# Kernel optimization log

Hardware: AMD Instinct MI355X
Metric: run time of the kernel (lower is better)

## Reference

```python
import jax, jax.numpy as jnp
import numpy as np

B, T, DC, DM, R = 64, 1000, 512, 80, 1
DP = 128          # prenet output dim
DH = 128          # prenet hidden dim
DA = 128          # attention hidden dim
DR = (1024, 1024) # decoder LSTM hidden dims
PZ = 0.1          # zoneout prob (eval-mode mixing)
PD = 0.5          # prenet dropout prob (always on)


def setup_inputs() -> dict:
    key = jax.random.key(0)
    ks = jax.random.split(key, 24)
    s = 0.02  # weight scale to keep activations in a sane range
    inp = {}
    inp['x'] = jax.random.normal(ks[0], (B, R, DM), jnp.float32)
    w = jax.random.uniform(ks[1], (B, T), jnp.float32)
    inp['w'] = w / jnp.sum(w, axis=1, keepdims=True)  # valid attention weights
    inp['h0'] = jax.random.normal(ks[2], (B, DR[0]), jnp.float32) * 0.1
    inp['c0'] = jax.random.normal(ks[3], (B, DR[0]), jnp.float32) * 0.1
    inp['h1'] = jax.random.normal(ks[4], (B, DR[1]), jnp.float32) * 0.1
    inp['c1'] = jax.random.normal(ks[5], (B, DR[1]), jnp.float32) * 0.1
    inp['memory'] = jax.random.normal(ks[6], (B, T, DC), jnp.float32)
    inp['mmask'] = jnp.ones((B, T), dtype=bool)
    inp['pre_w1'] = jax.random.normal(ks[7], (DM * R, DH), jnp.float32) * s
    inp['pre_b1'] = jnp.zeros((DH,), jnp.float32)
    inp['pre_w2'] = jax.random.normal(ks[8], (DH, DP), jnp.float32) * s
    inp['pre_b2'] = jnp.zeros((DP,), jnp.float32)
    inp['wih0'] = jax.random.normal(ks[9], (DP + DC, 4 * DR[0]), jnp.float32) * s
    inp['whh0'] = jax.random.normal(ks[10], (DR[0], 4 * DR[0]), jnp.float32) * s
    inp['b0'] = jnp.zeros((4 * DR[0],), jnp.float32)
    inp['wih1'] = jax.random.normal(ks[11], (DR[0] + DC, 4 * DR[1]), jnp.float32) * s
    inp['whh1'] = jax.random.normal(ks[12], (DR[1], 4 * DR[1]), jnp.float32) * s
    inp['b1'] = jnp.zeros((4 * DR[1],), jnp.float32)
    inp['att_wq'] = jax.random.normal(ks[13], (DR[0] + DR[1] + DC, DA), jnp.float32) * s
    inp['att_wm'] = jax.random.normal(ks[14], (DC, DA), jnp.float32) * s
    inp['att_b'] = jnp.zeros((DA,), jnp.float32)
    inp['att_v'] = jax.random.normal(ks[15], (DA,), jnp.float32) * s
    return inp


def _dropout(v, k, p):
    keep = jax.random.bernoulli(k, 1.0 - p, v.shape)
    return jnp.where(keep, v / (1.0 - p), 0.0)


def _lstm_zoneout(xi, h, c, wih, whh, b):
    # torch LSTMCell gate order: i, f, g, o
    g = xi @ wih + h @ whh + b
    i, f, gg, o = jnp.split(g, 4, axis=1)
    c_new = jax.nn.sigmoid(f) * c + jax.nn.sigmoid(i) * jnp.tanh(gg)
    h_new = jax.nn.sigmoid(o) * jnp.tanh(c_new)
    # eval-mode zoneout: expected-value mixing with previous state
    return (1.0 - PZ) * h_new + PZ * h, (1.0 - PZ) * c_new + PZ * c


def reference(x, w, h0, c0, h1, c1, memory, pre_w1, pre_b1, pre_w2, pre_b2,
              wih0, whh0, b0, wih1, whh1, b1, att_wq, att_wm, att_b, att_v, mmask):
    dk = jax.random.split(jax.random.key(42), 2)
    # PreNet (dropout always on, fixed keys for determinism)
    xf = x.reshape(x.shape[0], -1)                       # [B, r*dim_mel]
    h = _dropout(jax.nn.relu(xf @ pre_w1 + pre_b1), dk[0], PD)
    x_pre = _dropout(jax.nn.relu(h @ pre_w2 + pre_b2), dk[1], PD)  # [B, DP]
    # context = bmm(w, memory)
    ctx = jnp.einsum('bt,btc->bc', w, memory)            # [B, DC]
    # stacked zoneout LSTM cells with interleaved context concat
    h0n, c0n = _lstm_zoneout(jnp.concatenate([x_pre, ctx], axis=1), h0, c0, wih0, whh0, b0)
    h1n, c1n = _lstm_zoneout(jnp.concatenate([h0n, ctx], axis=1), h1, c1, wih1, whh1, b1)
    x_att = jnp.concatenate([h0n, h1n, jnp.zeros_like(ctx)], axis=1)  # [B, 2560]
    # stepwise monotonic attention: e = v.tanh(Wq q + Wm m + b); p = sigmoid(e)
    q = x_att @ att_wq                                   # [B, DA]
    proc = jnp.tanh(q[:, None, :] + jnp.einsum('btc,ca->bta', memory, att_wm) + att_b)
    e = jnp.einsum('bta,a->bt', proc, att_v)             # [B, T]
    e = jnp.where(mmask, e, -1e9)
    p = jax.nn.sigmoid(e)
    # alpha_j = alpha_j * p_j + alpha_{j-1} * (1 - p_{j-1})
    w_new = w * p + jnp.pad((w * (1.0 - p))[:, :-1], ((0, 0), (1, 0)))
    x_dec = jnp.concatenate([h0n, h1n, jnp.zeros_like(ctx)], axis=1)
    return x_dec, ctx, w_new, h0n, c0n, h1n, c1n
```

## Files before the change

### kernel.cpp

```cpp
#include <hip/hip_runtime.h>
#include <hip/hip_bf16.h>
#include <stdint.h>

#define B_  64
#define T_  1000
#define DC_ 512
#define DM_ 80
#define DP_ 128
#define DH_ 128
#define DA_ 128
#define DRN 1024
#define G4  4096

typedef __hip_bfloat16 bf16;
typedef unsigned short u16;
typedef unsigned int   u32;

typedef short bf8_t __attribute__((ext_vector_type(8)));
typedef float f4_t  __attribute__((ext_vector_type(4)));

#define O_XDEC 0
#define O_CTX  163840
#define O_WN   196608
#define O_H0   260608
#define O_C0   326144
#define O_H1   391680
#define O_C1   457216

__device__ __forceinline__ float b2f(bf16 v) { return __bfloat162float(v); }
__device__ __forceinline__ bf16  f2b(float v) { return __float2bfloat16(v); }
__device__ __forceinline__ u16   f2bu(float v) { return __builtin_bit_cast(u16, __float2bfloat16(v)); }

__device__ __forceinline__ float ldv(const float* p, size_t i) { return p[i]; }
__device__ __forceinline__ float ldv(const bf16*  p, size_t i) { return b2f(p[i]); }
__device__ __forceinline__ void  stv(float* p, size_t i, float v) { p[i] = v; }
__device__ __forceinline__ void  stv(bf16*  p, size_t i, float v) { p[i] = f2b(v); }

template<typename T>
__device__ __forceinline__ uint4 ld8bf(const T* p, size_t i) {
    if constexpr (sizeof(T) == 2) {
        return *(const uint4*)((const u16*)p + i);
    } else {
        float4 a = *(const float4*)(p + i);
        float4 b = *(const float4*)(p + i + 4);
        uint4 r;
        r.x = (u32)f2bu(a.x) | ((u32)f2bu(a.y) << 16);
        r.y = (u32)f2bu(a.z) | ((u32)f2bu(a.w) << 16);
        r.z = (u32)f2bu(b.x) | ((u32)f2bu(b.y) << 16);
        r.w = (u32)f2bu(b.z) | ((u32)f2bu(b.w) << 16);
        return r;
    }
}
template<typename T>
__device__ __forceinline__ void ld8f(const T* p, size_t i, float* o) {
    if constexpr (sizeof(T) == 2) {
        uint4 u = *(const uint4*)((const u16*)p + i);
        o[0] = __uint_as_float(u.x << 16); o[1] = __uint_as_float(u.x & 0xffff0000u);
        o[2] = __uint_as_float(u.y << 16); o[3] = __uint_as_float(u.y & 0xffff0000u);
        o[4] = __uint_as_float(u.z << 16); o[5] = __uint_as_float(u.z & 0xffff0000u);
        o[6] = __uint_as_float(u.w << 16); o[7] = __uint_as_float(u.w & 0xffff0000u);
    } else {
        float4 a = *(const float4*)(p + i);
        float4 b = *(const float4*)(p + i + 4);
        o[0]=a.x; o[1]=a.y; o[2]=a.z; o[3]=a.w; o[4]=b.x; o[5]=b.y; o[6]=b.z; o[7]=b.w;
    }
}
__device__ __forceinline__ void ld8f_bits(const u16* p, size_t i, float* o) {
    uint4 u = *(const uint4*)(p + i);
    o[0] = __uint_as_float(u.x << 16); o[1] = __uint_as_float(u.x & 0xffff0000u);
    o[2] = __uint_as_float(u.y << 16); o[3] = __uint_as_float(u.y & 0xffff0000u);
    o[4] = __uint_as_float(u.z << 16); o[5] = __uint_as_float(u.z & 0xffff0000u);
    o[6] = __uint_as_float(u.w << 16); o[7] = __uint_as_float(u.w & 0xffff0000u);
}

__device__ __forceinline__ bool sniff_is_f32(const u32* h0raw) {
    int lane = threadIdx.x & 63;
    int c = 0;
    #pragma unroll
    for (int i = 0; i < 4; ++i) {
        u32 e = (h0raw[lane * 4 + i] >> 7) & 0xFF;
        c += (e >= 100 && e <= 126) ? 1 : 0;
    }
    #pragma unroll
    for (int s = 1; s < 64; s <<= 1) c += __shfl_xor(c, s);
    return c < 128;
}

__device__ __forceinline__ u32 rotl32(u32 v, int r) { return (v << r) | (v >> (32 - r)); }
__device__ __forceinline__ void threefry2x32(u32 k0, u32 k1, u32 x0, u32 x1, u32& y0, u32& y1) {
    u32 ks2 = k0 ^ k1 ^ 0x1BD11BDAu;
    x0 += k0; x1 += k1;
#define TF_R(r) { x0 += x1; x1 = rotl32(x1, r); x1 ^= x0; }
    TF_R(13) TF_R(15) TF_R(26) TF_R(6)
    x0 += k1; x1 += ks2 + 1u;
    TF_R(17) TF_R(29) TF_R(16) TF_R(24)
    x0 += ks2; x1 += k0 + 2u;
    TF_R(13) TF_R(15) TF_R(26) TF_R(6)
    x0 += k0; x1 += k1 + 3u;
    TF_R(17) TF_R(29) TF_R(16) TF_R(24)
    x0 += k1; x1 += ks2 + 4u;
    TF_R(13) TF_R(15) TF_R(26) TF_R(6)
    x0 += ks2; x1 += k0 + 5u;
#undef TF_R
    y0 = x0; y1 = x1;
}
__device__ __forceinline__ float dropout_mask(int which, int j) {
    u32 dk0, dk1, b1, b2;
    threefry2x32(0u, 42u, 0u, (u32)which, dk0, dk1);
    threefry2x32(dk0, dk1, 0u, (u32)j, b1, b2);
    u32 bits = b1 ^ b2;
    float u = __uint_as_float((bits >> 9) | 0x3f800000u) - 1.0f;
    return (u < 0.5f) ? 2.0f : 0.0f;
}

template<typename T>
__device__ void prep_impl(const T* wm, const T* wq, u16* BTwm, u16* BTwq,
                          const T* x, const T* w1, const T* pb1, const T* w2, const T* pb2,
                          u16* Ab0, float* shbuf) {
    int bid = blockIdx.x, tid = threadIdx.x;
    if (bid < 160) {
        int gid = bid * 256 + tid;
        const T* src; u16* dst; int L, kc, at;
        if (gid < 8192) { L = gid & 63; kc = (gid >> 6) & 15; at = gid >> 10; src = wm; dst = BTwm + (size_t)gid * 8; }
        else { int g = gid - 8192; L = g & 63; kc = (g >> 6) & 63; at = g >> 12; src = wq; dst = BTwq + (size_t)g * 8; }
        int col = at * 16 + (L & 15);
        int krow = kc * 32 + (L >> 4) * 8;
        u16 v[8];
        #pragma unroll
        for (int j = 0; j < 8; ++j) v[j] = f2bu(ldv(src, (size_t)(krow + j) * DA_ + col));
        uint4 pk;
        pk.x = v[0] | ((u32)v[1] << 16); pk.y = v[2] | ((u32)v[3] << 16);
        pk.z = v[4] | ((u32)v[5] << 16); pk.w = v[6] | ((u32)v[7] << 16);
        *(uint4*)dst = pk;
    } else {
        int b = bid - 160;
        float* xs = shbuf;
        float* hs = shbuf + DM_;
        if (tid < DM_) xs[tid] = ldv(x, (size_t)b * DM_ + tid);
        __syncthreads();
        if (tid < DH_) {
            float acc = ldv(pb1, tid);
            #pragma unroll 8
            for (int k = 0; k < DM_; ++k) acc = fmaf(xs[k], ldv(w1, (size_t)k * DH_ + tid), acc);
            acc = fmaxf(acc, 0.f) * dropout_mask(0, b * DH_ + tid);
            hs[tid] = acc;
        }
        __syncthreads();
        if (tid < DP_) {
            float acc2 = ldv(pb2, tid);
            #pragma unroll 8
            for (int k = 0; k < DH_; ++k) acc2 = fmaf(hs[k], ldv(w2, (size_t)k * DP_ + tid), acc2);
            acc2 = fmaxf(acc2, 0.f) * dropout_mask(1, b * DP_ + tid);
            Ab0[(size_t)b * 1664 + tid] = f2bu(acc2);
        }
    }
}
__global__ __launch_bounds__(256) void prep_kernel(const u32* h0r,
        const void* wm, const void* wq, u16* BTwm, u16* BTwq,
        const void* x, const void* w1, const void* pb1, const void* w2, const void* pb2,
        u16* Ab0) {
    __shared__ float shbuf[DM_ + DH_];
    if (sniff_is_f32(h0r))
        prep_impl<float>((const float*)wm, (const float*)wq, BTwm, BTwq, (const float*)x,
                         (const float*)w1, (const float*)pb1, (const float*)w2, (const float*)pb2, Ab0, shbuf);
    else
        prep_impl<bf16>((const bf16*)wm, (const bf16*)wq, BTwm, BTwq, (const bf16*)x,
                        (const bf16*)w1, (const bf16*)pb1, (const bf16*)w2, (const bf16*)pb2, Ab0, shbuf);
}

template<typename T>
__device__ void ctxproj_impl(const T* mem, const T* w, const u16* BTwm,
                             float* CTXP, u16* Mproj, u16* Alds, float* shw) {
    int tid = threadIdx.x;
    int t0 = blockIdx.x * 128, b = blockIdx.y;
    if (tid < 128) shw[tid] = (t0 + tid < T_) ? ldv(w, (size_t)b * T_ + t0 + tid) : 0.f;
    int L = tid & 63;
    int m = L & 15, q16 = L >> 4;
    int wat = tid >> 6;
    int rg = tid >> 5, cg = tid & 31;

    bf8_t bw[16];
    #pragma unroll
    for (int kc = 0; kc < 16; ++kc)
        bw[kc] = *(const bf8_t*)(BTwm + ((size_t)(wat * 16 + kc) * 64 + L) * 8);

    f4_t acc[4];
    #pragma unroll
    for (int mt = 0; mt < 4; ++mt) acc[mt] = (f4_t){0.f, 0.f, 0.f, 0.f};
    float cacc[16] = {};
    uint4  stb[4];
    float4 stf[8];

#define LOADSTEP(S) do {                                                         \
        const int tt_ = (S) >> 1, ph_ = (S) & 1;                                 \
        _Pragma("unroll")                                                        \
        for (int rr = 0; rr < 4; ++rr) {                                         \
            int i = rr * 512 + tid;                                              \
            int row = i >> 5, c16 = i & 31;                                      \
            int t = t0 + tt_ * 64 + row;                                         \
            size_t base = (size_t)(b * T_ + ((t < T_) ? t : 0)) * DC_ + ph_ * 256 + c16 * 8; \
            if constexpr (sizeof(T) == 2) {                                      \
                stb[rr] = (t < T_) ? *(const uint4*)((const u16*)mem + base)     \
                                   : make_uint4(0u, 0u, 0u, 0u);                 \
            } else {                                                             \
                if (t < T_) { stf[2*rr]   = *(const float4*)(mem + base);        \
                              stf[2*rr+1] = *(const float4*)(mem + base + 4); }  \
                else { stf[2*rr] = make_float4(0.f,0.f,0.f,0.f);                 \
                       stf[2*rr+1] = make_float4(0.f,0.f,0.f,0.f); }             \
            }                                                                    \
        }                                                                        \
    } while (0)

    LOADSTEP(0);
    #pragma unroll
    for (int step = 0; step < 4; ++step) {
        const int tt = step >> 1, ph = step & 1;
        __syncthreads();
        #pragma unroll
        for (int rr = 0; rr < 4; ++rr) {
            int i = rr * 512 + tid;
            int row = i >> 5, c16 = i & 31;
            uint4 v;
            if constexpr (sizeof(T) == 2) {
                v = stb[rr];
            } else {
                float4 a = stf[2*rr], bb = stf[2*rr+1];
                v.x = (u32)f2bu(a.x)  | ((u32)f2bu(a.y)  << 16);
                v.y = (u32)f2bu(a.z)  | ((u32)f2bu(a.w)  << 16);
                v.z = (u32)f2bu(bb.x) | ((u32)f2bu(bb.y) << 16);
                v.w = (u32)f2bu(bb.z) | ((u32)f2bu(bb.w) << 16);
            }
            *(uint4*)(Alds + row * 264 + c16 * 8) = v;
        }
        __syncthreads();
        if (step == 0) LOADSTEP(1);
        else if (step == 1) LOADSTEP(2);
        else if (step == 2) LOADSTEP(3);
        #pragma unroll
        for (int rr = 0; rr < 4; ++rr) {
            int row = rg * 4 + rr;
            float v[8];
            ld8f_bits((const u16*)Alds, (size_t)row * 264 + cg * 8, v);
            float wvv = shw[tt * 64 + row];
            #pragma unroll
            for (int j = 0; j < 8; ++j) cacc[ph * 8 + j] = fmaf(wvv, v[j], cacc[ph * 8 + j]);
        }
        #pragma unroll
        for (int kcl = 0; kcl < 8; ++kcl) {
            const int kc = ph * 8 + kcl;
            #pragma unroll
            for (int mt = 0; mt < 4; ++mt) {
                bf8_t af = *(const bf8_t*)(Alds + (mt * 16 + m) * 264 + kcl * 32 + q16 * 8);
                acc[mt] = __builtin_amdgcn_mfma_f32_16x16x32_bf16(af, bw[kc], acc[mt], 0, 0, 0);
            }
        }
        if (ph == 1) {
            #pragma unroll
            for (int mt = 0; mt < 4; ++mt) {
                #pragma unroll
                for (int r = 0; r < 4; ++r) {
                    int trow = t0 + tt * 64 + mt * 16 + q16 * 4 + r;
                    if (trow < T_)
                        Mproj[(size_t)(b * T_ + trow) * DA_ + wat * 16 + m] = f2bu(acc[mt][r]);
                }
                acc[mt] = (f4_t){0.f, 0.f, 0.f, 0.f};
            }
        }
    }
#undef LOADSTEP
    __syncthreads();
    float* part = (float*)Alds;
    #pragma unroll
    for (int ph = 0; ph < 2; ++ph)
        #pragma unroll
        for (int j = 0; j < 8; ++j)
            part[rg * 512 + ph * 256 + cg * 8 + j] = cacc[ph * 8 + j];
    __syncthreads();
    int c = tid;
    float s = 0.f;
    #pragma unroll
    for (int gg = 0; gg < 16; ++gg) s += part[gg * 512 + c];
    CTXP[((size_t)blockIdx.x * 64 + b) * DC_ + c] = s;
}
__global__ __launch_bounds__(512, 1) void ctxproj_bf16_kernel(const u32* h0r,
        const void* mem, const void* w, const u16* BTwm, float* CTXP, u16* Mproj) {
    __shared__ __align__(16) u16 Alds[64 * 264];
    __shared__ float shw[128];
    if (sniff_is_f32(h0r)) return;
    ctxproj_impl<bf16>((const bf16*)mem, (const bf16*)w, BTwm, CTXP, Mproj, Alds, shw);
}
__global__ __launch_bounds__(512, 1) void ctxproj_f32_kernel(const u32* h0r,
        const void* mem, const void* w, const u16* BTwm, float* CTXP, u16* Mproj) {
    __shared__ __align__(16) u16 Alds[64 * 264];
    __shared__ float shw[128];
    if (!sniff_is_f32(h0r)) return;
    ctxproj_impl<float>((const float*)mem, (const float*)w, BTwm, CTXP, Mproj, Alds, shw);
}

template<typename T>
__device__ void pack0_impl(const float* CTXP, const T* h0p, const T* h1p,
                           u16* Ab0, u16* Ab1, T* out) {
    int b = blockIdx.x, tid = threadIdx.x;
    T* ctxout = out + O_CTX;
    T* xdec = out + O_XDEC;
    for (int c = tid; c < DC_; c += 256) {
        float s = 0.f;
        #pragma unroll
        for (int t = 0; t < 8; ++t) s += CTXP[((size_t)t * 64 + b) * DC_ + c];
        u16 bv = f2bu(s);
        Ab0[(size_t)b * 1664 + 128 + c] = bv;
        Ab1[(size_t)b * 2560 + 1024 + c] = bv;
        stv(ctxout, (size_t)b * DC_ + c, s);
        stv(xdec, (size_t)b * 2560 + 2048 + c, 0.f);
    }
    for (int u = tid; u < DRN; u += 256) {
        Ab0[(size_t)b * 1664 + 640 + u]  = f2bu(ldv(h0p, (size_t)b * DRN + u));
        Ab1[(size_t)b * 2560 + 1536 + u] = f2bu(ldv(h1p, (size_t)b * DRN + u));
    }
}
__global__ __launch_bounds__(256) void pack0_kernel(const u32* h0r, const float* CTXP,
        const void* h0p, const void* h1p, u16* Ab0, u16* Ab1, void* out) {
    if (sniff_is_f32(h0r))
        pack0_impl<float>(CTXP, (const float*)h0p, (const float*)h1p, Ab0, Ab1, (float*)out);
    else
        pack0_impl<bf16>(CTXP, (const bf16*)h0p, (const bf16*)h1p, Ab0, Ab1, (bf16*)out);
}

template<typename T>
__device__ void gemm_impl(const u16* Abuf, int K, int L12, const T* Wih, const T* Whh,
                          float* Gs, int nchunks, float (*As)[34], float (*Ws)[64]) {
    int tid = threadIdx.x;
    int n0b = blockIdx.x * 64;
    int kbase = blockIdx.y * (nchunks * 32);
    int cx = tid & 15, ry = tid >> 4;
    int b0 = ry * 4, n0 = cx * 4;
    int a_bb = tid >> 2, a_k8 = (tid & 3) * 8;
    int w_k  = tid >> 3, w_n8 = (tid & 7) * 8;
    float acc[4][4] = {};
    float va[8], vw[8];
    {
        int k0 = kbase;
        ld8f_bits(Abuf, (size_t)a_bb * K + k0 + a_k8, va);
        int kg = k0 + w_k;
        const T* wr = (kg < L12) ? (Wih + (size_t)kg * G4) : (Whh + (size_t)(kg - L12) * G4);
        ld8f(wr, n0b + w_n8, vw);
    }
    for (int ch = 0; ch < nchunks; ++ch) {
        __syncthreads();
        #pragma unroll
        for (int j = 0; j < 8; ++j) As[a_bb][a_k8 + j] = va[j];
        #pragma unroll
        for (int j = 0; j < 8; ++j) Ws[w_k][w_n8 + j] = vw[j];
        __syncthreads();
        if (ch + 1 < nchunks) {
            int k0 = kbase + (ch + 1) * 32;
            ld8f_bits(Abuf, (size_t)a_bb * K + k0 + a_k8, va);
            int kg = k0 + w_k;
            const T* wr = (kg < L12) ? (Wih + (size_t)kg * G4) : (Whh + (size_t)(kg - L12) * G4);
            ld8f(wr, n0b + w_n8, vw);
        }
        #pragma unroll
        for (int kk = 0; kk < 32; kk += 2) {
            float2 av[4];
            #pragma unroll
            for (int r = 0; r < 4; ++r) av[r] = *(const float2*)&As[b0 + r][kk];
            float4 w0 = *(const float4*)&Ws[kk][n0];
            float4 w1 = *(const float4*)&Ws[kk + 1][n0];
            #pragma unroll
            for (int r = 0; r < 4; ++r) {
                acc[r][0] = fmaf(av[r].x, w0.x, acc[r][0]); acc[r][0] = fmaf(av[r].y, w1.x, acc[r][0]);
                acc[r][1] = fmaf(av[r].x, w0.y, acc[r][1]); acc[r][1] = fmaf(av[r].y, w1.y, acc[r][1]);
                acc[r][2] = fmaf(av[r].x, w0.z, acc[r][2]); acc[r][2] = fmaf(av[r].y, w1.z, acc[r][2]);
                acc[r][3] = fmaf(av[r].x, w0.w, acc[r][3]); acc[r][3] = fmaf(av[r].y, w1.w, acc[r][3]);
            }
        }
    }
    float* outp = Gs + (size_t)blockIdx.y * (64 * G4);
    #pragma unroll
    for (int r = 0; r < 4; ++r)
        *(float4*)&outp[(size_t)(b0 + r) * G4 + n0b + n0] =
            make_float4(acc[r][0], acc[r][1], acc[r][2], acc[r][3]);
}
__global__ __launch_bounds__(256) void gemm_kernel(const u32* h0r, const u16* Abuf,
        int K, int L12, const void* Wih, const void* Whh, float* Gs, int nchunks) {
    __shared__ float As[64][34];
    __shared__ float Ws[32][64];
    if (sniff_is_f32(h0r))
        gemm_impl<float>(Abuf, K, L12, (const float*)Wih, (const float*)Whh, Gs, nchunks, As, Ws);
    else
        gemm_impl<bf16>(Abuf, K, L12, (const bf16*)Wih, (const bf16*)Whh, Gs, nchunks, As, Ws);
}

template<typename T>
__device__ void gate_impl(const float* Gs, int nsplit, const T* bias, const T* hprev,
                          const T* cprev, T* out, int ho_off, int co_off, int xoff,
                          u16* Hcat, int hoff, u16* Ab1) {
    int idx = blockIdx.x * 256 + threadIdx.x;
    int b = idx >> 10, u = idx & 1023;
    float gi = ldv(bias, u);
    float gf = ldv(bias, 1024 + u);
    float gg = ldv(bias, 2048 + u);
    float go = ldv(bias, 3072 + u);
    for (int s = 0; s < nsplit; ++s) {
        const float* g = Gs + (size_t)s * (64 * G4) + (size_t)b * G4;
        gi += g[u]; gf += g[1024 + u]; gg += g[2048 + u]; go += g[3072 + u];
    }
    float c = ldv(cprev, idx), h = ldv(hprev, idx);
    float si = 1.f / (1.f + expf(-gi));
    float sf = 1.f / (1.f + expf(-gf));
    float so = 1.f / (1.f + expf(-go));
    float cn = sf * c + si * tanhf(gg);
    float hn = so * tanhf(cn);
    float ho = 0.9f * hn + 0.1f * h;
    float co = 0.9f * cn + 0.1f * c;
    stv(out + ho_off, idx, ho);
    stv(out + co_off, idx, co);
    stv(out + O_XDEC, (size_t)b * 2560 + xoff + u, ho);
    u16 hb = f2bu(ho);
    Hcat[(size_t)b * 2048 + hoff + u] = hb;
    if (Ab1 != nullptr) Ab1[(size_t)b * 2560 + u] = hb;
}
__global__ __launch_bounds__(256) void gate_kernel(const u32* h0r, const float* Gs, int nsplit,
        const void* bias, const void* hprev, const void* cprev, void* out,
        int ho_off, int co_off, int xoff, u16* Hcat, int hoff, u16* Ab1) {
    if (sniff_is_f32(h0r))
        gate_impl<float>(Gs, nsplit, (const float*)bias, (const float*)hprev, (const float*)cprev,
                         (float*)out, ho_off, co_off, xoff, Hcat, hoff, Ab1);
    else
        gate_impl<bf16>(Gs, nsplit, (const bf16*)bias, (const bf16*)hprev, (const bf16*)cprev,
                        (bf16*)out, ho_off, co_off, xoff, Hcat, hoff, Ab1);
}

__global__ __launch_bounds__(256) void qgemm_kernel(const u16* Hcat, const u16* BTwq, float* QP) {
    int tid = threadIdx.x;
    int w = tid >> 6, L = tid & 63;
    int m = L & 15, q16 = L >> 4;
    f4_t acc[8];
    #pragma unroll
    for (int at = 0; at < 8; ++at) acc[at] = (f4_t){0.f, 0.f, 0.f, 0.f};
    #pragma unroll
    for (int kcl = 0; kcl < 8; ++kcl) {
        int kc = blockIdx.x * 8 + kcl;
        bf8_t af = *(const bf8_t*)(Hcat + (size_t)(w * 16 + m) * 2048 + kc * 32 + q16 * 8);
        #pragma unroll
        for (int at = 0; at < 8; ++at) {
            bf8_t bfrag = *(const bf8_t*)(BTwq + ((size_t)(at * 64 + kc) * 64 + L) * 8);
            acc[at] = __builtin_amdgcn_mfma_f32_16x16x32_bf16(af, bfrag, acc[at], 0, 0, 0);
        }
    }
    #pragma unroll
    for (int at = 0; at < 8; ++at)
        #pragma unroll
        for (int r = 0; r < 4; ++r)
            QP[((size_t)blockIdx.x * 64 + w * 16 + q16 * 4 + r) * DA_ + at * 16 + m] = acc[at][r];
}

template<typename T>
__device__ void attn_impl(const u16* Mproj, const float* QP, const T* ab, const T* av,
                          const T* w, T* out, float* qa, float* avl, float* psh) {
    int tid = threadIdx.x;
    int t0 = blockIdx.x * 64, b = blockIdx.y;
    T* wout = out + O_WN;
    if (tid < DA_) {
        float s = ldv(ab, tid);
        #pragma unroll
        for (int s8 = 0; s8 < 8; ++s8) s += QP[((size_t)s8 * 64 + b) * DA_ + tid];
        qa[tid] = s;
        avl[tid] = ldv(av, tid);
    }
    __syncthreads();
    int quad = tid & 3, r = tid >> 2;
    #pragma unroll
    for (int rbase = 0; rbase < 2; ++rbase) {
        int rrow = (rbase == 0) ? r : 64;
        bool act = (rbase == 0) || (r == 0);
        int t = t0 - 1 + rrow;
        float e = 0.f;
        if (act && t >= 0 && t < T_) {
            #pragma unroll
            for (int a8 = 0; a8 < 4; ++a8) {
                float v[8];
                ld8f_bits(Mproj, (size_t)(b * T_ + t) * DA_ + quad * 32 + a8 * 8, v);
                #pragma unroll
                for (int j = 0; j < 8; ++j) {
                    int a = quad * 32 + a8 * 8 + j;
                    e = fmaf(avl[a], tanhf(qa[a] + v[j]), e);
                }
            }
        }
        e += __shfl_xor(e, 1);
        e += __shfl_xor(e, 2);
        if (act && quad == 0 && t >= 0 && t < T_) psh[rrow] = 1.f / (1.f + expf(-e));
    }
    __syncthreads();
    if (tid < 64) {
        int t = t0 + tid;
        if (t < T_) {
            float val = ldv(w, (size_t)b * T_ + t) * psh[tid + 1];
            if (t > 0) val = fmaf(ldv(w, (size_t)b * T_ + t - 1), 1.f - psh[tid], val);
            stv(wout, (size_t)b * T_ + t, val);
        }
    }
}
__global__ __launch_bounds__(256) void attn_kernel(const u32* h0r, const u16* Mproj,
        const float* QP, const void* ab, const void* av, const void* w, void* out) {
    __shared__ float qa[DA_];
    __shared__ float avl[DA_];
    __shared__ float psh[66];
    if (sniff_is_f32(h0r))
        attn_impl<float>(Mproj, QP, (const float*)ab, (const float*)av, (const float*)w,
                         (float*)out, qa, avl, psh);
    else
        attn_impl<bf16>(Mproj, QP, (const bf16*)ab, (const bf16*)av, (const bf16*)w,
                        (bf16*)out, qa, avl, psh);
}

extern "C" void kernel_launch(void* const* d_in, const int* in_sizes, int n_in,
                              void* d_out, int out_size, void* d_ws, size_t ws_size,
                              hipStream_t stream) {
    (void)in_sizes; (void)n_in; (void)out_size; (void)ws_size;

    float* wsf   = (float*)d_ws;
    float* GS    = wsf;
    float* CTXP  = wsf + 4194304;
    float* QP    = wsf + 4718592;
    u16*   MPROJ = (u16*)(wsf + 4784128);
    u16*   AB0   = (u16*)(wsf + 8880128);
    u16*   AB1   = (u16*)(wsf + 8933376);
    u16*   HCAT  = (u16*)(wsf + 9015296);
    u16*   BTWM  = (u16*)(wsf + 9080832);
    u16*   BTWQ  = (u16*)(wsf + 9113600);

    const u32* H0R = (const u32*)d_in[2];

    prep_kernel<<<224, 256, 0, stream>>>(H0R, d_in[19], d_in[18], BTWM, BTWQ,
                                         d_in[0], d_in[8], d_in[9], d_in[10], d_in[11], AB0);
    ctxproj_bf16_kernel<<<dim3(8, 64), 512, 0, stream>>>(H0R, d_in[6], d_in[1], BTWM, CTXP, MPROJ);
    ctxproj_f32_kernel <<<dim3(8, 64), 512, 0, stream>>>(H0R, d_in[6], d_in[1], BTWM, CTXP, MPROJ);
    pack0_kernel<<<64, 256, 0, stream>>>(H0R, CTXP, d_in[2], d_in[4], AB0, AB1, d_out);
    gemm_kernel<<<dim3(64, 13), 256, 0, stream>>>(H0R, AB0, 1664, 640, d_in[12], d_in[13], GS, 4);
    gate_kernel<<<256, 256, 0, stream>>>(H0R, GS, 13, d_in[14], d_in[2], d_in[3], d_out,
                                         O_H0, O_C0, 0, HCAT, 0, AB1);
    gemm_kernel<<<dim3(64, 16), 256, 0, stream>>>(H0R, AB1, 2560, 1536, d_in[15], d_in[16], GS, 5);
    gate_kernel<<<256, 256, 0, stream>>>(H0R, GS, 16, d_in[17], d_in[4], d_in[5], d_out,
                                         O_H1, O_C1, 1024, HCAT, 1024, (u16*)nullptr);
    qgemm_kernel<<<8, 256, 0, stream>>>(HCAT, BTWQ, QP);
    attn_kernel<<<dim3(16, 64), 256, 0, stream>>>(H0R, MPROJ, QP, d_in[20], d_in[21], d_in[1], d_out);
}
```

Baseline: 389.5 us.

## Fuse query projection into gate kernels, widen GEMM K-chunks, fold context FMA into staging

The separate qgemm kernel and its Wq repack are removed. Each gate kernel now computes a partial query projection from its freshly computed hidden units and atomically accumulates it into a zeroed buffer that the attention kernel reads directly. The LSTM GEMM K-chunk grows from 32 to 64, with the split grid shrunk accordingly for layer 1 from 16 to 10 splits. The context weighted-sum is folded into the register staging path instead of re-reading from LDS. This trades one launch and a repack for float atomics, uncoalesced fp32 Wq reads inside the gate kernel, and fewer, longer GEMM blocks.

```diff
diff --git a/kernel.cpp b/kernel.cpp
--- a/kernel.cpp
+++ b/kernel.cpp
@@ -36,21 +36,6 @@
 __device__ __forceinline__ void  stv(float* p, size_t i, float v) { p[i] = v; }
 __device__ __forceinline__ void  stv(bf16*  p, size_t i, float v) { p[i] = f2b(v); }
 
-template<typename T>
-__device__ __forceinline__ uint4 ld8bf(const T* p, size_t i) {
-    if constexpr (sizeof(T) == 2) {
-        return *(const uint4*)((const u16*)p + i);
-    } else {
-        float4 a = *(const float4*)(p + i);
-        float4 b = *(const float4*)(p + i + 4);
-        uint4 r;
-        r.x = (u32)f2bu(a.x) | ((u32)f2bu(a.y) << 16);
-        r.y = (u32)f2bu(a.z) | ((u32)f2bu(a.w) << 16);
-        r.z = (u32)f2bu(b.x) | ((u32)f2bu(b.y) << 16);
-        r.w = (u32)f2bu(b.z) | ((u32)f2bu(b.w) << 16);
-        return r;
-    }
-}
 template<typename T>
 __device__ __forceinline__ void ld8f(const T* p, size_t i, float* o) {
     if constexpr (sizeof(T) == 2) {
@@ -114,26 +99,25 @@
 }
 
 template<typename T>
-__device__ void prep_impl(const T* wm, const T* wq, u16* BTwm, u16* BTwq,
+__device__ void prep_impl(const T* wm, u16* BTwm,
                           const T* x, const T* w1, const T* pb1, const T* w2, const T* pb2,
                           u16* Ab0, float* shbuf) {
     int bid = blockIdx.x, tid = threadIdx.x;
-    if (bid < 160) {
+    if (bid < 32) {
         int gid = bid * 256 + tid;
-        const T* src; u16* dst; int L, kc, at;
-        if (gid < 8192) { L = gid & 63; kc = (gid >> 6) & 15; at = gid >> 10; src = wm; dst = BTwm + (size_t)gid * 8; }
-        else { int g = gid - 8192; L = g & 63; kc = (g >> 6) & 63; at = g >> 12; src = wq; dst = BTwq + (size_t)g * 8; }
+        int L = gid & 63, kc = (gid >> 6) & 15, at = gid >> 10;
+        u16* dst = BTwm + (size_t)gid * 8;
         int col = at * 16 + (L & 15);
         int krow = kc * 32 + (L >> 4) * 8;
         u16 v[8];
         #pragma unroll
-        for (int j = 0; j < 8; ++j) v[j] = f2bu(ldv(src, (size_t)(krow + j) * DA_ + col));
+        for (int j = 0; j < 8; ++j) v[j] = f2bu(ldv(wm, (size_t)(krow + j) * DA_ + col));
         uint4 pk;
         pk.x = v[0] | ((u32)v[1] << 16); pk.y = v[2] | ((u32)v[3] << 16);
         pk.z = v[4] | ((u32)v[5] << 16); pk.w = v[6] | ((u32)v[7] << 16);
         *(uint4*)dst = pk;
     } else {
-        int b = bid - 160;
+        int b = bid - 32;
         float* xs = shbuf;
         float* hs = shbuf + DM_;
         if (tid < DM_) xs[tid] = ldv(x, (size_t)b * DM_ + tid);
@@ -156,15 +140,15 @@
     }
 }
 __global__ __launch_bounds__(256) void prep_kernel(const u32* h0r,
-        const void* wm, const void* wq, u16* BTwm, u16* BTwq,
+        const void* wm, u16* BTwm,
         const void* x, const void* w1, const void* pb1, const void* w2, const void* pb2,
         u16* Ab0) {
     __shared__ float shbuf[DM_ + DH_];
     if (sniff_is_f32(h0r))
-        prep_impl<float>((const float*)wm, (const float*)wq, BTwm, BTwq, (const float*)x,
+        prep_impl<float>((const float*)wm, BTwm, (const float*)x,
                          (const float*)w1, (const float*)pb1, (const float*)w2, (const float*)pb2, Ab0, shbuf);
     else
-        prep_impl<bf16>((const bf16*)wm, (const bf16*)wq, BTwm, BTwq, (const bf16*)x,
+        prep_impl<bf16>((const bf16*)wm, BTwm, (const bf16*)x,
                         (const bf16*)w1, (const bf16*)pb1, (const bf16*)w2, (const bf16*)pb2, Ab0, shbuf);
 }
 
@@ -220,11 +204,24 @@
         for (int rr = 0; rr < 4; ++rr) {
             int i = rr * 512 + tid;
             int row = i >> 5, c16 = i & 31;
+            float wvv = shw[tt * 64 + row];
             uint4 v;
             if constexpr (sizeof(T) == 2) {
                 v = stb[rr];
+                float f0 = __uint_as_float(v.x << 16), f1 = __uint_as_float(v.x & 0xffff0000u);
+                float f2 = __uint_as_float(v.y << 16), f3 = __uint_as_float(v.y & 0xffff0000u);
+                float f4 = __uint_as_float(v.z << 16), f5 = __uint_as_float(v.z & 0xffff0000u);
+                float f6 = __uint_as_float(v.w << 16), f7 = __uint_as_float(v.w & 0xffff0000u);
+                cacc[ph*8+0] = fmaf(wvv, f0, cacc[ph*8+0]); cacc[ph*8+1] = fmaf(wvv, f1, cacc[ph*8+1]);
+                cacc[ph*8+2] = fmaf(wvv, f2, cacc[ph*8+2]); cacc[ph*8+3] = fmaf(wvv, f3, cacc[ph*8+3]);
+                cacc[ph*8+4] = fmaf(wvv, f4, cacc[ph*8+4]); cacc[ph*8+5] = fmaf(wvv, f5, cacc[ph*8+5]);
+                cacc[ph*8+6] = fmaf(wvv, f6, cacc[ph*8+6]); cacc[ph*8+7] = fmaf(wvv, f7, cacc[ph*8+7]);
             } else {
                 float4 a = stf[2*rr], bb = stf[2*rr+1];
+                cacc[ph*8+0] = fmaf(wvv, a.x,  cacc[ph*8+0]); cacc[ph*8+1] = fmaf(wvv, a.y,  cacc[ph*8+1]);
+                cacc[ph*8+2] = fmaf(wvv, a.z,  cacc[ph*8+2]); cacc[ph*8+3] = fmaf(wvv, a.w,  cacc[ph*8+3]);
+                cacc[ph*8+4] = fmaf(wvv, bb.x, cacc[ph*8+4]); cacc[ph*8+5] = fmaf(wvv, bb.y, cacc[ph*8+5]);
+                cacc[ph*8+6] = fmaf(wvv, bb.z, cacc[ph*8+6]); cacc[ph*8+7] = fmaf(wvv, bb.w, cacc[ph*8+7]);
                 v.x = (u32)f2bu(a.x)  | ((u32)f2bu(a.y)  << 16);
                 v.y = (u32)f2bu(a.z)  | ((u32)f2bu(a.w)  << 16);
                 v.z = (u32)f2bu(bb.x) | ((u32)f2bu(bb.y) << 16);
@@ -236,15 +233,6 @@
         if (step == 0) LOADSTEP(1);
         else if (step == 1) LOADSTEP(2);
         else if (step == 2) LOADSTEP(3);
-        #pragma unroll
-        for (int rr = 0; rr < 4; ++rr) {
-            int row = rg * 4 + rr;
-            float v[8];
-            ld8f_bits((const u16*)Alds, (size_t)row * 264 + cg * 8, v);
-            float wvv = shw[tt * 64 + row];
-            #pragma unroll
-            for (int j = 0; j < 8; ++j) cacc[ph * 8 + j] = fmaf(wvv, v[j], cacc[ph * 8 + j]);
-        }
         #pragma unroll
         for (int kcl = 0; kcl < 8; ++kcl) {
             const int kc = ph * 8 + kcl;
@@ -299,10 +287,11 @@
 
 template<typename T>
 __device__ void pack0_impl(const float* CTXP, const T* h0p, const T* h1p,
-                           u16* Ab0, u16* Ab1, T* out) {
+                           u16* Ab0, u16* Ab1, float* QPf, T* out) {
     int b = blockIdx.x, tid = threadIdx.x;
     T* ctxout = out + O_CTX;
     T* xdec = out + O_XDEC;
+    if (tid < 128) QPf[(size_t)b * DA_ + tid] = 0.f;
     for (int c = tid; c < DC_; c += 256) {
         float s = 0.f;
         #pragma unroll
@@ -319,48 +308,45 @@
     }
 }
 __global__ __launch_bounds__(256) void pack0_kernel(const u32* h0r, const float* CTXP,
-        const void* h0p, const void* h1p, u16* Ab0, u16* Ab1, void* out) {
+        const void* h0p, const void* h1p, u16* Ab0, u16* Ab1, float* QPf, void* out) {
     if (sniff_is_f32(h0r))
-        pack0_impl<float>(CTXP, (const float*)h0p, (const float*)h1p, Ab0, Ab1, (float*)out);
+        pack0_impl<float>(CTXP, (const float*)h0p, (const float*)h1p, Ab0, Ab1, QPf, (float*)out);
     else
-        pack0_impl<bf16>(CTXP, (const bf16*)h0p, (const bf16*)h1p, Ab0, Ab1, (bf16*)out);
+        pack0_impl<bf16>(CTXP, (const bf16*)h0p, (const bf16*)h1p, Ab0, Ab1, QPf, (bf16*)out);
 }
 
 template<typename T>
 __device__ void gemm_impl(const u16* Abuf, int K, int L12, const T* Wih, const T* Whh,
-                          float* Gs, int nchunks, float (*As)[34], float (*Ws)[64]) {
+                          float* Gs, int nchunks, float (*As)[66], float (*Ws)[64]) {
     int tid = threadIdx.x;
     int n0b = blockIdx.x * 64;
-    int kbase = blockIdx.y * (nchunks * 32);
+    int kbase = blockIdx.y * (nchunks * 64);
     int cx = tid & 15, ry = tid >> 4;
     int b0 = ry * 4, n0 = cx * 4;
-    int a_bb = tid >> 2, a_k8 = (tid & 3) * 8;
-    int w_k  = tid >> 3, w_n8 = (tid & 7) * 8;
+    int a_bb = tid >> 2, a_k16 = (tid & 3) * 16;
+    int w_k  = tid >> 2, w_n16 = (tid & 3) * 16;
     float acc[4][4] = {};
-    float va[8], vw[8];
-    {
-        int k0 = kbase;
-        ld8f_bits(Abuf, (size_t)a_bb * K + k0 + a_k8, va);
-        int kg = k0 + w_k;
-        const T* wr = (kg < L12) ? (Wih + (size_t)kg * G4) : (Whh + (size_t)(kg - L12) * G4);
-        ld8f(wr, n0b + w_n8, vw);
-    }
+    float va[16], vw[16];
+#define GLOAD(CH) do {                                                          \
+        int k0 = kbase + (CH) * 64;                                             \
+        ld8f_bits(Abuf, (size_t)a_bb * K + k0 + a_k16, va);                     \
+        ld8f_bits(Abuf, (size_t)a_bb * K + k0 + a_k16 + 8, va + 8);             \
+        int kg = k0 + w_k;                                                      \
+        const T* wr = (kg < L12) ? (Wih + (size_t)kg * G4) : (Whh + (size_t)(kg - L12) * G4); \
+        ld8f(wr, n0b + w_n16, vw);                                              \
+        ld8f(wr, n0b + w_n16 + 8, vw + 8);                                      \
+    } while (0)
+    GLOAD(0);
     for (int ch = 0; ch < nchunks; ++ch) {
         __syncthreads();
         #pragma unroll
-        for (int j = 0; j < 8; ++j) As[a_bb][a_k8 + j] = va[j];
-        #pragma unroll
-        for (int j = 0; j < 8; ++j) Ws[w_k][w_n8 + j] = vw[j];
+        for (int j = 0; j < 16; ++j) As[a_bb][a_k16 + j] = va[j];
+        #pragma unroll
+        for (int j = 0; j < 16; ++j) Ws[w_k][w_n16 + j] = vw[j];
         __syncthreads();
-        if (ch + 1 < nchunks) {
-            int k0 = kbase + (ch + 1) * 32;
-            ld8f_bits(Abuf, (size_t)a_bb * K + k0 + a_k8, va);
-            int kg = k0 + w_k;
-            const T* wr = (kg < L12) ? (Wih + (size_t)kg * G4) : (Whh + (size_t)(kg - L12) * G4);
-            ld8f(wr, n0b + w_n8, vw);
-        }
-        #pragma unroll
-        for (int kk = 0; kk < 32; kk += 2) {
+        if (ch + 1 < nchunks) GLOAD(ch + 1);
+        #pragma unroll
+        for (int kk = 0; kk < 64; kk += 2) {
             float2 av[4];
             #pragma unroll
             for (int r = 0; r < 4; ++r) av[r] = *(const float2*)&As[b0 + r][kk];
@@ -375,6 +361,7 @@
             }
         }
     }
+#undef GLOAD
     float* outp = Gs + (size_t)blockIdx.y * (64 * G4);
     #pragma unroll
     for (int r = 0; r < 4; ++r)
@@ -383,8 +370,8 @@
 }
 __global__ __launch_bounds__(256) void gemm_kernel(const u32* h0r, const u16* Abuf,
         int K, int L12, const void* Wih, const void* Whh, float* Gs, int nchunks) {
-    __shared__ float As[64][34];
-    __shared__ float Ws[32][64];
+    __shared__ float As[64][66];
+    __shared__ float Ws[64][64];
     if (sniff_is_f32(h0r))
         gemm_impl<float>(Abuf, K, L12, (const float*)Wih, (const float*)Whh, Gs, nchunks, As, Ws);
     else
@@ -393,10 +380,13 @@
 
 template<typename T>
 __device__ void gate_impl(const float* Gs, int nsplit, const T* bias, const T* hprev,
-                          const T* cprev, T* out, int ho_off, int co_off, int xoff,
-                          u16* Hcat, int hoff, u16* Ab1) {
-    int idx = blockIdx.x * 256 + threadIdx.x;
+                          const T* cprev, const T* wq, int qrow0, float* QPf,
+                          T* out, int ho_off, int co_off, int xoff, u16* Ab1,
+                          float* hos, float* sarr) {
+    int tid = threadIdx.x;
+    int idx = blockIdx.x * 256 + tid;
     int b = idx >> 10, u = idx & 1023;
+    int u0 = (blockIdx.x & 3) * 256;
     float gi = ldv(bias, u);
     float gf = ldv(bias, 1024 + u);
     float gg = ldv(bias, 2048 + u);
@@ -416,56 +406,39 @@
     stv(out + ho_off, idx, ho);
     stv(out + co_off, idx, co);
     stv(out + O_XDEC, (size_t)b * 2560 + xoff + u, ho);
-    u16 hb = f2bu(ho);
-    Hcat[(size_t)b * 2048 + hoff + u] = hb;
-    if (Ab1 != nullptr) Ab1[(size_t)b * 2560 + u] = hb;
+    if (Ab1 != nullptr) Ab1[(size_t)b * 2560 + u] = f2bu(ho);
+    hos[tid] = ho;
+    __syncthreads();
+    int a = tid & 127, half = tid >> 7;
+    float s = 0.f;
+    #pragma unroll 8
+    for (int j = 0; j < 128; ++j)
+        s = fmaf(hos[half * 128 + j], ldv(wq, (size_t)(qrow0 + u0 + half * 128 + j) * DA_ + a), s);
+    sarr[tid] = s;
+    __syncthreads();
+    if (tid < 128) atomicAdd(&QPf[(size_t)b * DA_ + tid], sarr[tid] + sarr[128 + tid]);
 }
 __global__ __launch_bounds__(256) void gate_kernel(const u32* h0r, const float* Gs, int nsplit,
-        const void* bias, const void* hprev, const void* cprev, void* out,
-        int ho_off, int co_off, int xoff, u16* Hcat, int hoff, u16* Ab1) {
+        const void* bias, const void* hprev, const void* cprev, const void* wq, int qrow0,
+        float* QPf, void* out, int ho_off, int co_off, int xoff, u16* Ab1) {
+    __shared__ float hos[256];
+    __shared__ float sarr[256];
     if (sniff_is_f32(h0r))
         gate_impl<float>(Gs, nsplit, (const float*)bias, (const float*)hprev, (const float*)cprev,
-                         (float*)out, ho_off, co_off, xoff, Hcat, hoff, Ab1);
+                         (const float*)wq, qrow0, QPf, (float*)out, ho_off, co_off, xoff, Ab1, hos, sarr);
     else
         gate_impl<bf16>(Gs, nsplit, (const bf16*)bias, (const bf16*)hprev, (const bf16*)cprev,
-                        (bf16*)out, ho_off, co_off, xoff, Hcat, hoff, Ab1);
-}
-
-__global__ __launch_bounds__(256) void qgemm_kernel(const u16* Hcat, const u16* BTwq, float* QP) {
-    int tid = threadIdx.x;
-    int w = tid >> 6, L = tid & 63;
-    int m = L & 15, q16 = L >> 4;
-    f4_t acc[8];
-    #pragma unroll
-    for (int at = 0; at < 8; ++at) acc[at] = (f4_t){0.f, 0.f, 0.f, 0.f};
-    #pragma unroll
-    for (int kcl = 0; kcl < 8; ++kcl) {
-        int kc = blockIdx.x * 8 + kcl;
-        bf8_t af = *(const bf8_t*)(Hcat + (size_t)(w * 16 + m) * 2048 + kc * 32 + q16 * 8);
-        #pragma unroll
-        for (int at = 0; at < 8; ++at) {
-            bf8_t bfrag = *(const bf8_t*)(BTwq + ((size_t)(at * 64 + kc) * 64 + L) * 8);
-            acc[at] = __builtin_amdgcn_mfma_f32_16x16x32_bf16(af, bfrag, acc[at], 0, 0, 0);
-        }
-    }
-    #pragma unroll
-    for (int at = 0; at < 8; ++at)
-        #pragma unroll
-        for (int r = 0; r < 4; ++r)
-            QP[((size_t)blockIdx.x * 64 + w * 16 + q16 * 4 + r) * DA_ + at * 16 + m] = acc[at][r];
-}
-
-template<typename T>
-__device__ void attn_impl(const u16* Mproj, const float* QP, const T* ab, const T* av,
+                        (const bf16*)wq, qrow0, QPf, (bf16*)out, ho_off, co_off, xoff, Ab1, hos, sarr);
+}
+
+template<typename T>
+__device__ void attn_impl(const u16* Mproj, const float* QPf, const T* ab, const T* av,
                           const T* w, T* out, float* qa, float* avl, float* psh) {
     int tid = threadIdx.x;
     int t0 = blockIdx.x * 64, b = blockIdx.y;
     T* wout = out + O_WN;
     if (tid < DA_) {
-        float s = ldv(ab, tid);
-        #pragma unroll
-        for (int s8 = 0; s8 < 8; ++s8) s += QP[((size_t)s8 * 64 + b) * DA_ + tid];
-        qa[tid] = s;
+        qa[tid]  = ldv(ab, tid) + QPf[(size_t)b * DA_ + tid];
         avl[tid] = ldv(av, tid);
     }
     __syncthreads();
@@ -503,15 +476,15 @@
     }
 }
 __global__ __launch_bounds__(256) void attn_kernel(const u32* h0r, const u16* Mproj,
-        const float* QP, const void* ab, const void* av, const void* w, void* out) {
+        const float* QPf, const void* ab, const void* av, const void* w, void* out) {
     __shared__ float qa[DA_];
     __shared__ float avl[DA_];
     __shared__ float psh[66];
     if (sniff_is_f32(h0r))
-        attn_impl<float>(Mproj, QP, (const float*)ab, (const float*)av, (const float*)w,
+        attn_impl<float>(Mproj, QPf, (const float*)ab, (const float*)av, (const float*)w,
                          (float*)out, qa, avl, psh);
     else
-        attn_impl<bf16>(Mproj, QP, (const bf16*)ab, (const bf16*)av, (const bf16*)w,
+        attn_impl<bf16>(Mproj, QPf, (const bf16*)ab, (const bf16*)av, (const bf16*)w,
                         (bf16*)out, qa, avl, psh);
 }
 
@@ -523,27 +496,24 @@
     float* wsf   = (float*)d_ws;
     float* GS    = wsf;
     float* CTXP  = wsf + 4194304;
-    float* QP    = wsf + 4718592;
+    float* QPf   = wsf + 4718592;
     u16*   MPROJ = (u16*)(wsf + 4784128);
     u16*   AB0   = (u16*)(wsf + 8880128);
     u16*   AB1   = (u16*)(wsf + 8933376);
-    u16*   HCAT  = (u16*)(wsf + 9015296);
     u16*   BTWM  = (u16*)(wsf + 9080832);
-    u16*   BTWQ  = (u16*)(wsf + 9113600);
 
     const u32* H0R = (const u32*)d_in[2];
 
-    prep_kernel<<<224, 256, 0, stream>>>(H0R, d_in[19], d_in[18], BTWM, BTWQ,
-                                         d_in[0], d_in[8], d_in[9], d_in[10], d_in[11], AB0);
+    prep_kernel<<<96, 256, 0, stream>>>(H0R, d_in[19], BTWM,
+                                        d_in[0], d_in[8], d_in[9], d_in[10], d_in[11], AB0);
     ctxproj_bf16_kernel<<<dim3(8, 64), 512, 0, stream>>>(H0R, d_in[6], d_in[1], BTWM, CTXP, MPROJ);
     ctxproj_f32_kernel <<<dim3(8, 64), 512, 0, stream>>>(H0R, d_in[6], d_in[1], BTWM, CTXP, MPROJ);
-    pack0_kernel<<<64, 256, 0, stream>>>(H0R, CTXP, d_in[2], d_in[4], AB0, AB1, d_out);
-    gemm_kernel<<<dim3(64, 13), 256, 0, stream>>>(H0R, AB0, 1664, 640, d_in[12], d_in[13], GS, 4);
-    gate_kernel<<<256, 256, 0, stream>>>(H0R, GS, 13, d_in[14], d_in[2], d_in[3], d_out,
-                                         O_H0, O_C0, 0, HCAT, 0, AB1);
-    gemm_kernel<<<dim3(64, 16), 256, 0, stream>>>(H0R, AB1, 2560, 1536, d_in[15], d_in[16], GS, 5);
-    gate_kernel<<<256, 256, 0, stream>>>(H0R, GS, 16, d_in[17], d_in[4], d_in[5], d_out,
-                                         O_H1, O_C1, 1024, HCAT, 1024, (u16*)nullptr);
-    qgemm_kernel<<<8, 256, 0, stream>>>(HCAT, BTWQ, QP);
-    attn_kernel<<<dim3(16, 64), 256, 0, stream>>>(H0R, MPROJ, QP, d_in[20], d_in[21], d_in[1], d_out);
-}
+    pack0_kernel<<<64, 256, 0, stream>>>(H0R, CTXP, d_in[2], d_in[4], AB0, AB1, QPf, d_out);
+    gemm_kernel<<<dim3(64, 13), 256, 0, stream>>>(H0R, AB0, 1664, 640, d_in[12], d_in[13], GS, 2);
+    gate_kernel<<<256, 256, 0, stream>>>(H0R, GS, 13, d_in[14], d_in[2], d_in[3],
+                                         d_in[18], 0, QPf, d_out, O_H0, O_C0, 0, AB1);
+    gemm_kernel<<<dim3(64, 10), 256, 0, stream>>>(H0R, AB1, 2560, 1536, d_in[15], d_in[16], GS, 4);
+    gate_kernel<<<256, 256, 0, stream>>>(H0R, GS, 10, d_in[17], d_in[4], d_in[5],
+                                         d_in[18], 1024, QPf, d_out, O_H1, O_C1, 1024, (u16*)nullptr);
+    attn_kernel<<<dim3(16, 64), 256, 0, stream>>>(H0R, MPROJ, QPf, d_in[20], d_in[21], d_in[1], d_out);
+}
```

Measured after the change: 384.5 us. No clear change (-1.3%).
